# Performance work log

Measured on AMD Instinct MI355X. Metric: run time of the kernel, lower is better.

## Reference

```python
import jax, jax.numpy as jnp
import numpy as np

B, L, D = 8, 4096, 512
KS = (3, 5, 7)
EPS = 1e-5
W_SCALE = 0.02  # tame torch.randn-style init for numerical sanity


def layernorm(x, g, b):
    mu = jnp.mean(x, axis=-1, keepdims=True)
    var = jnp.var(x, axis=-1, keepdims=True)
    return (x - mu) * jax.lax.rsqrt(var + EPS) * g + b


def masked_conv(x1, chain, W, b):
    # x1: (B, C, L); W: (O, C, K); chain: (B, L) int32
    K = W.shape[2]
    pad_l = (K - 1) // 2
    pad_r = (K - 1) - pad_l
    xp = jnp.pad(x1, ((0, 0), (0, 0), (pad_l, pad_r)))
    ip = jnp.pad(chain, ((0, 0), (pad_l, pad_r)))  # pad id = 0
    Lx = x1.shape[2]
    # center tap of each window is the position's own chain id (odd K, center == pad_l)
    out = b[None, :, None]
    for k in range(K):  # small static loop over taps
        xs = xp[:, :, k:k + Lx]                      # (B, C, L)
        mk = (ip[:, k:k + Lx] == chain)              # (B, L) bool
        out = out + jnp.einsum('bcl,oc->bol', xs * mk[:, None, :], W[:, :, k])
    return out


def setup_inputs() -> dict:
    key = jax.random.key(0)
    ks = jax.random.split(key, 16)
    inp = {
        'x': jax.random.normal(ks[0], (B, L, D), dtype=jnp.float32),
        'chain': jnp.sort(jax.random.randint(ks[1], (B, L), 0, 8), axis=-1).astype(jnp.int32),
    }
    for i, (name, K) in enumerate(zip(('W3', 'W5', 'W7'), KS)):
        inp[name] = jax.random.normal(ks[2 + i], (D, D, K), dtype=jnp.float32) * W_SCALE
        inp['b' + name[1:]] = jax.random.normal(ks[5 + i], (D,), dtype=jnp.float32) * W_SCALE
    inp['mlp_w1'] = jax.random.normal(ks[8], (D, 4 * D), dtype=jnp.float32) * W_SCALE
    inp['mlp_b1'] = jnp.zeros((4 * D,), dtype=jnp.float32)
    inp['mlp_w2'] = jax.random.normal(ks[9], (4 * D, D), dtype=jnp.float32) * W_SCALE
    inp['mlp_b2'] = jnp.zeros((D,), dtype=jnp.float32)
    inp['ln1_g'] = jnp.ones((D,), dtype=jnp.float32)
    inp['ln1_b'] = jnp.zeros((D,), dtype=jnp.float32)
    inp['ln2_g'] = jnp.ones((D,), dtype=jnp.float32)
    inp['ln2_b'] = jnp.zeros((D,), dtype=jnp.float32)
    return inp


def reference(x, chain, W3, b3, W5, b5, W7, b7,
              mlp_w1, mlp_b1, mlp_w2, mlp_b2,
              ln1_g, ln1_b, ln2_g, ln2_b):
    x1 = jnp.transpose(x, (0, 2, 1))  # (B, C, L)
    for W, b in ((W3, b3), (W5, b5), (W7, b7)):
        x1 = masked_conv(x1, chain, W, b)
    h = layernorm(x + jnp.transpose(x1, (0, 2, 1)), ln1_g, ln1_b)
    mlp = jax.nn.gelu(h @ mlp_w1 + mlp_b1) @ mlp_w2 + mlp_b2
    return layernorm(h + mlp, ln2_g, ln2_b)
```

## Files before the change

kernel.cpp:

```cpp
#include <hip/hip_runtime.h>
#include <math.h>

#define BB 8
#define LL 4096
#define DD 512
#define PTOT (BB*LL)
#define HID  2048

typedef __attribute__((ext_vector_type(8))) short short8;
typedef __attribute__((ext_vector_type(4))) float f32x4;

typedef __attribute__((address_space(1))) const unsigned int gconst_u32;
typedef __attribute__((address_space(3))) unsigned int lds_u32;

__device__ __forceinline__ void gload16(const void* g, void* l) {
    __builtin_amdgcn_global_load_lds((gconst_u32*)g, (lds_u32*)l, 16, 0, 0);
}

__device__ __forceinline__ unsigned short f2bf(float f) {
    union { float f; unsigned int u; } v; v.f = f;
    unsigned int r = v.u + 0x7fffu + ((v.u >> 16) & 1u);
    return (unsigned short)(r >> 16);
}
__device__ __forceinline__ float bf2f(unsigned short h) {
    union { unsigned int u; float f; } v; v.u = ((unsigned int)h) << 16;
    return v.f;
}
__device__ __forceinline__ float gelu_fast(float x) {
    float x2 = x * x;
    float t  = x * fmaf(0.044715f, x2, 1.0f);
    float e  = __builtin_amdgcn_exp2f(-2.3021143f * t);
    return x * __builtin_amdgcn_rcpf(1.0f + e);
}

__device__ __forceinline__ void barrier_sync() {
    asm volatile("" ::: "memory");
    __builtin_amdgcn_s_barrier();
    asm volatile("" ::: "memory");
}
#define WAITV(N) asm volatile("s_waitcnt vmcnt(" #N ")" ::: "memory")
#define WAITL0() asm volatile("s_waitcnt lgkmcnt(0)" ::: "memory")
#define SCHED0() __builtin_amdgcn_sched_barrier(0)

__global__ __launch_bounds__(256) void convert_x(const float* __restrict__ x,
                                                 unsigned short* __restrict__ xb,
                                                 unsigned short* __restrict__ zp) {
    int tid = blockIdx.x * 256 + threadIdx.x;
    if (blockIdx.x == 0 && threadIdx.x < 128) zp[threadIdx.x] = 0;
    float4 v = ((const float4*)x)[tid];
    uint2 o;
    o.x = (unsigned int)f2bf(v.x) | ((unsigned int)f2bf(v.y) << 16);
    o.y = (unsigned int)f2bf(v.z) | ((unsigned int)f2bf(v.w) << 16);
    ((uint2*)xb)[tid] = o;
}

__global__ __launch_bounds__(256) void trans_wconv(const float* __restrict__ W,
                                                   unsigned short* __restrict__ Wt, int K) {
    int tid = blockIdx.x * 256 + threadIdx.x;
    if (tid >= DD * DD * K) return;
    int o  = tid / (K * DD);
    int kc = tid - o * K * DD;
    int k  = kc >> 9;
    int c  = kc & (DD - 1);
    Wt[tid] = f2bf(W[(o * DD + c) * K + k]);
}

__global__ __launch_bounds__(256) void trans_w1(const float* __restrict__ W,
                                                unsigned short* __restrict__ Wt) {
    int tid = blockIdx.x * 256 + threadIdx.x;
    int n = tid >> 9;
    int c = tid & (DD - 1);
    Wt[tid] = f2bf(W[c * HID + n]);
}

__global__ __launch_bounds__(256) void trans_w2(const float* __restrict__ W,
                                                unsigned short* __restrict__ Wt) {
    int tid = blockIdx.x * 256 + threadIdx.x;
    int n = tid >> 11;
    int h = tid & (HID - 1);
    Wt[tid] = f2bf(W[h * DD + n]);
}

__global__ __launch_bounds__(256) void make_srcp(const int* __restrict__ chain,
                                                 int* __restrict__ srcp, int K) {
    int tid = blockIdx.x * 256 + threadIdx.x;
    if (tid >= PTOT * K) return;
    int p = tid / K;
    int k = tid - p * K;
    int b = p >> 12;
    int l = p & (LL - 1);
    int pad = (K - 1) >> 1;
    int l2 = l + k - pad;
    bool ok = (l2 >= 0) && (l2 < LL) && (chain[b * LL + l2] == chain[b * LL + l]);
    srcp[tid] = ok ? (p + k - pad) : -1;
}

template <int TAPS, int EPI>
__global__ __launch_bounds__(512) void mfma_gemm6(
        const unsigned short* __restrict__ A, int lda,
        const int* __restrict__ srcp,
        const unsigned short* __restrict__ Bt, int ldb,
        const float* __restrict__ bias,
        void* __restrict__ Yv, int ldc, int Kspan,
        const unsigned short* __restrict__ zp) {
    __shared__ alignas(16) unsigned short As[2 * 256 * 64];
    __shared__ alignas(16) unsigned short Bs[2 * 256 * 64];
    __shared__ int srcp_s[TAPS > 0 ? 256 * TAPS : 4];

    const int t = threadIdx.x;
    const int lane = t & 63, w = t >> 6;
    const int wr = w & 1, wc = w >> 1;
    const int lm = lane & 15, qh = lane >> 4, x7 = lane & 7;
    const int qq = (lane & 7) ^ (lane >> 3);
    const int l3 = lane >> 3;
    const int p0 = blockIdx.x * 256;
    const int o0 = blockIdx.y * 256;
    const int NKT = TAPS ? TAPS * 8 : (Kspan >> 6);

    f32x4 acc[8][4];
#pragma unroll
    for (int mi = 0; mi < 8; mi++)
#pragma unroll
        for (int nj = 0; nj < 4; nj++) acc[mi][nj] = (f32x4){0.f, 0.f, 0.f, 0.f};

    auto stgB = [&](int h) {
        if (h >= 4 * NKT) return;
        int jt = h >> 2;
        int rb = (h & 2) ? 128 : 0;
        unsigned short* dst = Bs + (jt & 1) * 16384 + (rb + w * 16) * 64;
        int kb = jt << 6;
#pragma unroll
        for (int i = 0; i < 2; i++) {
            int rl = rb + w * 16 + i * 8 + l3;
            gload16(Bt + (size_t)(o0 + rl) * ldb + kb + qq * 8, dst + i * 512);
        }
    };
    auto stgA = [&](int h, int sp0, int sp1) {
        if (h >= 4 * NKT) return;
        int jt = h >> 2;
        int rb = (h & 2) ? 128 : 0;
        unsigned short* dst = As + (jt & 1) * 16384 + (rb + w * 16) * 64;
#pragma unroll
        for (int i = 0; i < 2; i++) {
            const unsigned short* g;
            if (TAPS) {
                int sp = i ? sp1 : sp0;
                g = (sp >= 0) ? (A + (size_t)sp * lda + (jt & 7) * 64 + qq * 8) : zp;
            } else {
                int rl = rb + w * 16 + i * 8 + l3;
                g = A + (size_t)(p0 + rl) * lda + (jt << 6) + qq * 8;
            }
            gload16(g, dst + i * 512);
        }
    };
    auto ldsp = [&](int h, int& sp0, int& sp1) {
        if (TAPS && h < 4 * NKT) {
            int jt = h >> 2, tap = jt >> 3;
            int rb = (h & 2) ? 128 : 0;
            int rl = rb + w * 16 + l3;
            sp0 = srcp_s[rl * TAPS + tap];
            sp1 = srcp_s[(rl + 8) * TAPS + tap];
        }
    };

    if (TAPS) {
        for (int idx = t; idx < 256 * TAPS; idx += 512)
            srcp_s[idx] = srcp[(size_t)p0 * TAPS + idx];
    }
    __syncthreads();
    int sp0 = -1, sp1 = -1;
    ldsp(0, sp0, sp1); stgA(0, sp0, sp1);
    stgB(1);
    ldsp(2, sp0, sp1); stgA(2, sp0, sp1);
    stgB(3);
    ldsp(4, sp0, sp1); stgA(4, sp0, sp1);
    stgB(5);
    ldsp(6, sp0, sp1);
    WAITV(4);
    barrier_sync();

#define RD_A(MIH) do {                                                          \
    _Pragma("unroll")                                                           \
    for (int kk = 0; kk < 2; kk++) {                                            \
        int sa = ((kk * 4 + qh) ^ x7) * 8;                                      \
        _Pragma("unroll")                                                       \
        for (int m = 0; m < 4; m++)                                             \
            af[m][kk] = *(const short8*)&as_[((((MIH)*4+m)*2 + wr)*16 + lm)*64 + sa]; \
    } } while (0)
#define RD_B(NJH, BF) do {                                                      \
    _Pragma("unroll")                                                           \
    for (int kk = 0; kk < 2; kk++) {                                            \
        int sa = ((kk * 4 + qh) ^ x7) * 8;                                      \
        _Pragma("unroll")                                                       \
        for (int n = 0; n < 2; n++)                                             \
            BF[n][kk] = *(const short8*)&bs_[((((NJH)*2+n)*4 + wc)*16 + lm)*64 + sa]; \
    } } while (0)
#define MFMA_Q(MIH, NJH, BF)                                                    \
    __builtin_amdgcn_s_setprio(1);                                              \
    _Pragma("unroll")                                                           \
    for (int kk = 0; kk < 2; kk++)                                              \
        _Pragma("unroll")                                                       \
        for (int m = 0; m < 4; m++)                                             \
            _Pragma("unroll")                                                   \
            for (int n = 0; n < 2; n++)                                         \
                acc[(MIH)*4+m][(NJH)*2+n] = __builtin_amdgcn_mfma_f32_16x16x32_bf16( \
                    af[m][kk], BF[n][kk], acc[(MIH)*4+m][(NJH)*2+n], 0, 0, 0);  \
    __builtin_amdgcn_s_setprio(0)

    short8 af[4][2], bf0[2][2], bf1[2][2];
#pragma unroll 1
    for (int kt = 0; kt < NKT; ++kt) {
        const unsigned short* as_ = As + (kt & 1) * 16384;
        const unsigned short* bs_ = Bs + (kt & 1) * 16384;
        const bool last = (kt == NKT - 1);
        RD_A(0); RD_B(0, bf0); RD_B(1, bf1);
        if (!last) { stgA(4 * kt + 6, sp0, sp1); stgB(4 * kt + 7); }
        WAITL0(); SCHED0();
        MFMA_Q(0, 0, bf0);
        MFMA_Q(0, 1, bf1);
        if (!last) ldsp(4 * kt + 8, sp0, sp1);
        barrier_sync();
        RD_A(1);
        if (!last) { stgA(4 * kt + 8, sp0, sp1); stgB(4 * kt + 9); }
        WAITL0(); SCHED0();
        MFMA_Q(1, 0, bf0);
        MFMA_Q(1, 1, bf1);
        if (!last) ldsp(4 * kt + 10, sp0, sp1);
        if (kt == NKT - 2) { WAITV(0); } else if (!last) { WAITV(4); }
        barrier_sync();
    }
#undef RD_A
#undef RD_B
#undef MFMA_Q

#pragma unroll
    for (int mi = 0; mi < 8; mi++) {
#pragma unroll
        for (int nj = 0; nj < 4; nj++) {
            int col = o0 + (nj * 4 + wc) * 16 + lm;
#pragma unroll
            for (int r = 0; r < 4; r++) {
                int row = p0 + (mi * 2 + wr) * 16 + qh * 4 + r;
                float v = acc[mi][nj][r];
                size_t idx = (size_t)row * ldc + col;
                if (EPI == 0) {
                    ((unsigned short*)Yv)[idx] = f2bf(v + bias[col]);
                } else if (EPI == 1) {
                    ((unsigned short*)Yv)[idx] = f2bf(gelu_fast(v + bias[col]));
                } else if (EPI == 2) {
                    ((float*)Yv)[idx] = v + bias[col];
                } else {
                    ((float*)Yv)[idx] += v;
                }
            }
        }
    }
}

__global__ __launch_bounds__(256) void ln1_kernel(const float* __restrict__ x,
                                                  const unsigned short* __restrict__ conv,
                                                  const float* __restrict__ g,
                                                  const float* __restrict__ beta,
                                                  unsigned short* __restrict__ h) {
    int p = blockIdx.x, t = threadIdx.x;
    size_t base = (size_t)p * DD;
    float v0 = x[base + t] + bf2f(conv[base + t]);
    float v1 = x[base + 256 + t] + bf2f(conv[base + 256 + t]);
    float s = v0 + v1, sq = v0 * v0 + v1 * v1;
#pragma unroll
    for (int off = 32; off > 0; off >>= 1) { s += __shfl_xor(s, off); sq += __shfl_xor(sq, off); }
    __shared__ float red[2][4];
    int wid = t >> 6, lane = t & 63;
    if (lane == 0) { red[0][wid] = s; red[1][wid] = sq; }
    __syncthreads();
    float S = red[0][0] + red[0][1] + red[0][2] + red[0][3];
    float SQ = red[1][0] + red[1][1] + red[1][2] + red[1][3];
    float mu = S * (1.f / DD);
    float var = SQ * (1.f / DD) - mu * mu;
    float rs = rsqrtf(var + 1e-5f);
    h[base + t]       = f2bf((v0 - mu) * rs * g[t] + beta[t]);
    h[base + 256 + t] = f2bf((v1 - mu) * rs * g[256 + t] + beta[256 + t]);
}

__global__ __launch_bounds__(256) void ln2_kernel(const unsigned short* __restrict__ h,
                                                  float* __restrict__ out,
                                                  const float* __restrict__ g,
                                                  const float* __restrict__ beta) {
    int p = blockIdx.x, t = threadIdx.x;
    size_t base = (size_t)p * DD;
    float v0 = bf2f(h[base + t]) + out[base + t];
    float v1 = bf2f(h[base + 256 + t]) + out[base + 256 + t];
    float s = v0 + v1, sq = v0 * v0 + v1 * v1;
#pragma unroll
    for (int off = 32; off > 0; off >>= 1) { s += __shfl_xor(s, off); sq += __shfl_xor(sq, off); }
    __shared__ float red[2][4];
    int wid = t >> 6, lane = t & 63;
    if (lane == 0) { red[0][wid] = s; red[1][wid] = sq; }
    __syncthreads();
    float S = red[0][0] + red[0][1] + red[0][2] + red[0][3];
    float SQ = red[1][0] + red[1][1] + red[1][2] + red[1][3];
    float mu = S * (1.f / DD);
    float var = SQ * (1.f / DD) - mu * mu;
    float rs = rsqrtf(var + 1e-5f);
    out[base + t]       = (v0 - mu) * rs * g[t] + beta[t];
    out[base + 256 + t] = (v1 - mu) * rs * g[256 + t] + beta[256 + t];
}

extern "C" void kernel_launch(void* const* d_in, const int* in_sizes, int n_in,
                              void* d_out, int out_size, void* d_ws, size_t ws_size,
                              hipStream_t stream) {
    const float* x     = (const float*)d_in[0];
    const int*   chain = (const int*)d_in[1];
    const float* W3    = (const float*)d_in[2];
    const float* b3    = (const float*)d_in[3];
    const float* W5    = (const float*)d_in[4];
    const float* b5    = (const float*)d_in[5];
    const float* W7    = (const float*)d_in[6];
    const float* b7    = (const float*)d_in[7];
    const float* w1    = (const float*)d_in[8];
    const float* bm1   = (const float*)d_in[9];
    const float* w2    = (const float*)d_in[10];
    const float* bm2   = (const float*)d_in[11];
    const float* g1    = (const float*)d_in[12];
    const float* be1   = (const float*)d_in[13];
    const float* g2    = (const float*)d_in[14];
    const float* be2   = (const float*)d_in[15];
    float* out = (float*)d_out;

    const size_t ACT = (size_t)PTOT * DD * 2;
    char* ws = (char*)d_ws;
    size_t off = 0;
    unsigned short* Xb   = (unsigned short*)(ws + off); off += ACT;
    unsigned short* buf1 = (unsigned short*)(ws + off); off += ACT;
    unsigned short* buf2 = (unsigned short*)(ws + off); off += ACT;
    unsigned short* w3t  = (unsigned short*)(ws + off); off += (size_t)3 * DD * DD * 2;
    unsigned short* w5t  = (unsigned short*)(ws + off); off += (size_t)5 * DD * DD * 2;
    unsigned short* w7t  = (unsigned short*)(ws + off); off += (size_t)7 * DD * DD * 2;
    unsigned short* w1t  = (unsigned short*)(ws + off); off += (size_t)DD * HID * 2;
    unsigned short* w2t  = (unsigned short*)(ws + off); off += (size_t)DD * HID * 2;
    int* srcp3 = (int*)(ws + off); off += (size_t)PTOT * 3 * 4;
    int* srcp5 = (int*)(ws + off); off += (size_t)PTOT * 5 * 4;
    int* srcp7 = (int*)(ws + off); off += (size_t)PTOT * 7 * 4;
    unsigned short* zp = (unsigned short*)(ws + off); off += 256;
    size_t base_off = off;
    bool full = (ws_size >= base_off + (size_t)PTOT * HID * 2);
    unsigned short* Hb = (unsigned short*)(ws + base_off);

    convert_x<<<PTOT * DD / (256 * 4), 256, 0, stream>>>(x, Xb, zp);
    trans_wconv<<<(DD * DD * 3 + 255) / 256, 256, 0, stream>>>(W3, w3t, 3);
    trans_wconv<<<(DD * DD * 5 + 255) / 256, 256, 0, stream>>>(W5, w5t, 5);
    trans_wconv<<<(DD * DD * 7 + 255) / 256, 256, 0, stream>>>(W7, w7t, 7);
    trans_w1<<<DD * HID / 256, 256, 0, stream>>>(w1, w1t);
    trans_w2<<<DD * HID / 256, 256, 0, stream>>>(w2, w2t);
    make_srcp<<<(PTOT * 3 + 255) / 256, 256, 0, stream>>>(chain, srcp3, 3);
    make_srcp<<<(PTOT * 5 + 255) / 256, 256, 0, stream>>>(chain, srcp5, 5);
    make_srcp<<<(PTOT * 7 + 255) / 256, 256, 0, stream>>>(chain, srcp7, 7);

    dim3 gconv(PTOT / 256, DD / 256);

    mfma_gemm6<3, 0><<<gconv, 512, 0, stream>>>(Xb, DD, srcp3, w3t, 3 * DD, b3, buf1, DD, DD, zp);
    mfma_gemm6<5, 0><<<gconv, 512, 0, stream>>>(buf1, DD, srcp5, w5t, 5 * DD, b5, buf2, DD, DD, zp);
    mfma_gemm6<7, 0><<<gconv, 512, 0, stream>>>(buf2, DD, srcp7, w7t, 7 * DD, b7, buf1, DD, DD, zp);

    ln1_kernel<<<PTOT, 256, 0, stream>>>(x, buf1, g1, be1, buf2);

    if (full) {
        dim3 g1d(PTOT / 256, HID / 256);
        mfma_gemm6<0, 1><<<g1d, 512, 0, stream>>>(buf2, DD, nullptr, w1t, DD, bm1,
                                                  Hb, HID, DD, zp);
        mfma_gemm6<0, 2><<<gconv, 512, 0, stream>>>(Hb, HID, nullptr, w2t, HID, bm2,
                                                    out, DD, HID, zp);
    } else {
        for (int jc = 0; jc < 4; jc++) {
            mfma_gemm6<0, 1><<<gconv, 512, 0, stream>>>(buf2, DD, nullptr,
                                                        w1t + (size_t)jc * DD * DD, DD,
                                                        bm1 + jc * DD, Hb, DD, DD, zp);
            if (jc == 0)
                mfma_gemm6<0, 2><<<gconv, 512, 0, stream>>>(Hb, DD, nullptr,
                                                            w2t + jc * DD, HID, bm2,
                                                            out, DD, DD, zp);
            else
                mfma_gemm6<0, 3><<<gconv, 512, 0, stream>>>(Hb, DD, nullptr,
                                                            w2t + jc * DD, HID, bm2,
                                                            out, DD, DD, zp);
        }
    }

    ln2_kernel<<<PTOT, 256, 0, stream>>>(buf2, out, g2, be2);
}
```

Before: 652.7 us.

## Deepen GEMM prefetch pipeline and preload next-tile LDS fragments before barrier

Restructures the main MFMA GEMM loop so the first A/B fragments of the next k-tile are read from LDS at the end of each iteration, letting MFMAs start right after the barrier. Global-to-LDS staging now issues all four stages of the next tile at once, with a deeper vmcnt wait (8 outstanding loads instead of 4). The aim is to hide LDS read latency and global-load latency behind the MFMAs. In exchange it uses more registers for the extra srcp indices and relies on subtle barrier and wait-count correctness around the double-buffered LDS.

```diff
diff --git a/kernel.cpp b/kernel.cpp
--- a/kernel.cpp
+++ b/kernel.cpp
@@ -96,7 +96,7 @@
 }
 
 template <int TAPS, int EPI>
-__global__ __launch_bounds__(512) void mfma_gemm6(
+__global__ __launch_bounds__(512) void mfma_gemm8(
         const unsigned short* __restrict__ A, int lda,
         const int* __restrict__ srcp,
         const unsigned short* __restrict__ Bt, int ldb,
@@ -168,34 +168,31 @@
             srcp_s[idx] = srcp[(size_t)p0 * TAPS + idx];
     }
     __syncthreads();
-    int sp0 = -1, sp1 = -1;
-    ldsp(0, sp0, sp1); stgA(0, sp0, sp1);
-    stgB(1);
-    ldsp(2, sp0, sp1); stgA(2, sp0, sp1);
-    stgB(3);
-    ldsp(4, sp0, sp1); stgA(4, sp0, sp1);
-    stgB(5);
-    ldsp(6, sp0, sp1);
-    WAITV(4);
+    int sp0 = -1, sp1 = -1, sp2 = -1, sp3 = -1;
+    ldsp(0, sp0, sp1); stgA(0, sp0, sp1); stgB(1);
+    ldsp(2, sp0, sp1); stgA(2, sp0, sp1); stgB(3);
+    ldsp(4, sp0, sp1); stgA(4, sp0, sp1); stgB(5);
+    ldsp(6, sp0, sp1); stgA(6, sp0, sp1); stgB(7);
+    WAITV(8);
     barrier_sync();
 
-#define RD_A(MIH) do {                                                          \
+#define RD_A(AF, MIH, BASE) do {                                                \
     _Pragma("unroll")                                                           \
     for (int kk = 0; kk < 2; kk++) {                                            \
         int sa = ((kk * 4 + qh) ^ x7) * 8;                                      \
         _Pragma("unroll")                                                       \
         for (int m = 0; m < 4; m++)                                             \
-            af[m][kk] = *(const short8*)&as_[((((MIH)*4+m)*2 + wr)*16 + lm)*64 + sa]; \
+            AF[m][kk] = *(const short8*)&(BASE)[((((MIH)*4+m)*2 + wr)*16 + lm)*64 + sa]; \
     } } while (0)
-#define RD_B(NJH, BF) do {                                                      \
+#define RD_B(BF, NJH, BASE) do {                                                \
     _Pragma("unroll")                                                           \
     for (int kk = 0; kk < 2; kk++) {                                            \
         int sa = ((kk * 4 + qh) ^ x7) * 8;                                      \
         _Pragma("unroll")                                                       \
         for (int n = 0; n < 2; n++)                                             \
-            BF[n][kk] = *(const short8*)&bs_[((((NJH)*2+n)*4 + wc)*16 + lm)*64 + sa]; \
+            BF[n][kk] = *(const short8*)&(BASE)[((((NJH)*2+n)*4 + wc)*16 + lm)*64 + sa]; \
     } } while (0)
-#define MFMA_Q(MIH, NJH, BF)                                                    \
+#define MFMA_Q(AF, MIH, BF, NJH)                                                \
     __builtin_amdgcn_s_setprio(1);                                              \
     _Pragma("unroll")                                                           \
     for (int kk = 0; kk < 2; kk++)                                              \
@@ -204,29 +201,45 @@
             _Pragma("unroll")                                                   \
             for (int n = 0; n < 2; n++)                                         \
                 acc[(MIH)*4+m][(NJH)*2+n] = __builtin_amdgcn_mfma_f32_16x16x32_bf16( \
-                    af[m][kk], BF[n][kk], acc[(MIH)*4+m][(NJH)*2+n], 0, 0, 0);  \
+                    AF[m][kk], BF[n][kk], acc[(MIH)*4+m][(NJH)*2+n], 0, 0, 0);  \
     __builtin_amdgcn_s_setprio(0)
 
     short8 af[4][2], bf0[2][2], bf1[2][2];
+    RD_A(af, 0, As);
+    RD_B(bf0, 0, Bs);
+
 #pragma unroll 1
     for (int kt = 0; kt < NKT; ++kt) {
-        const unsigned short* as_ = As + (kt & 1) * 16384;
-        const unsigned short* bs_ = Bs + (kt & 1) * 16384;
+        const unsigned short* as_  = As + (kt & 1) * 16384;
+        const unsigned short* bs_  = Bs + (kt & 1) * 16384;
+        const unsigned short* as2_ = As + ((kt + 1) & 1) * 16384;
+        const unsigned short* bs2_ = Bs + ((kt + 1) & 1) * 16384;
         const bool last = (kt == NKT - 1);
-        RD_A(0); RD_B(0, bf0); RD_B(1, bf1);
-        if (!last) { stgA(4 * kt + 6, sp0, sp1); stgB(4 * kt + 7); }
-        WAITL0(); SCHED0();
-        MFMA_Q(0, 0, bf0);
-        MFMA_Q(0, 1, bf1);
-        if (!last) ldsp(4 * kt + 8, sp0, sp1);
+        RD_B(bf1, 1, bs_);
+        MFMA_Q(af, 0, bf0, 0);
+        MFMA_Q(af, 0, bf1, 1);
+        SCHED0();
+        RD_A(af, 1, as_);
+        if (!last) {
+            ldsp(4 * kt + 8, sp0, sp1);
+            ldsp(4 * kt + 10, sp2, sp3);
+            WAITV(4);
+        }
+        WAITL0();
         barrier_sync();
-        RD_A(1);
-        if (!last) { stgA(4 * kt + 8, sp0, sp1); stgB(4 * kt + 9); }
-        WAITL0(); SCHED0();
-        MFMA_Q(1, 0, bf0);
-        MFMA_Q(1, 1, bf1);
-        if (!last) ldsp(4 * kt + 10, sp0, sp1);
-        if (kt == NKT - 2) { WAITV(0); } else if (!last) { WAITV(4); }
+        MFMA_Q(af, 1, bf0, 0);
+        MFMA_Q(af, 1, bf1, 1);
+        SCHED0();
+        if (!last) {
+            RD_A(af, 0, as2_);
+            RD_B(bf0, 0, bs2_);
+            stgA(4 * kt + 8, sp0, sp1);
+            stgB(4 * kt + 9);
+            stgA(4 * kt + 10, sp2, sp3);
+            stgB(4 * kt + 11);
+            if (kt == NKT - 2) { WAITV(0); } else { WAITV(8); }
+        }
+        WAITL0();
         barrier_sync();
     }
 #undef RD_A
@@ -358,29 +371,29 @@
 
     dim3 gconv(PTOT / 256, DD / 256);
 
-    mfma_gemm6<3, 0><<<gconv, 512, 0, stream>>>(Xb, DD, srcp3, w3t, 3 * DD, b3, buf1, DD, DD, zp);
-    mfma_gemm6<5, 0><<<gconv, 512, 0, stream>>>(buf1, DD, srcp5, w5t, 5 * DD, b5, buf2, DD, DD, zp);
-    mfma_gemm6<7, 0><<<gconv, 512, 0, stream>>>(buf2, DD, srcp7, w7t, 7 * DD, b7, buf1, DD, DD, zp);
+    mfma_gemm8<3, 0><<<gconv, 512, 0, stream>>>(Xb, DD, srcp3, w3t, 3 * DD, b3, buf1, DD, DD, zp);
+    mfma_gemm8<5, 0><<<gconv, 512, 0, stream>>>(buf1, DD, srcp5, w5t, 5 * DD, b5, buf2, DD, DD, zp);
+    mfma_gemm8<7, 0><<<gconv, 512, 0, stream>>>(buf2, DD, srcp7, w7t, 7 * DD, b7, buf1, DD, DD, zp);
 
     ln1_kernel<<<PTOT, 256, 0, stream>>>(x, buf1, g1, be1, buf2);
 
     if (full) {
         dim3 g1d(PTOT / 256, HID / 256);
-        mfma_gemm6<0, 1><<<g1d, 512, 0, stream>>>(buf2, DD, nullptr, w1t, DD, bm1,
+        mfma_gemm8<0, 1><<<g1d, 512, 0, stream>>>(buf2, DD, nullptr, w1t, DD, bm1,
                                                   Hb, HID, DD, zp);
-        mfma_gemm6<0, 2><<<gconv, 512, 0, stream>>>(Hb, HID, nullptr, w2t, HID, bm2,
+        mfma_gemm8<0, 2><<<gconv, 512, 0, stream>>>(Hb, HID, nullptr, w2t, HID, bm2,
                                                     out, DD, HID, zp);
     } else {
         for (int jc = 0; jc < 4; jc++) {
-            mfma_gemm6<0, 1><<<gconv, 512, 0, stream>>>(buf2, DD, nullptr,
+            mfma_gemm8<0, 1><<<gconv, 512, 0, stream>>>(buf2, DD, nullptr,
                                                         w1t + (size_t)jc * DD * DD, DD,
                                                         bm1 + jc * DD, Hb, DD, DD, zp);
             if (jc == 0)
-                mfma_gemm6<0, 2><<<gconv, 512, 0, stream>>>(Hb, DD, nullptr,
+                mfma_gemm8<0, 2><<<gconv, 512, 0, stream>>>(Hb, DD, nullptr,
                                                             w2t + jc * DD, HID, bm2,
                                                             out, DD, DD, zp);
             else
-                mfma_gemm6<0, 3><<<gconv, 512, 0, stream>>>(Hb, DD, nullptr,
+                mfma_gemm8<0, 3><<<gconv, 512, 0, stream>>>(Hb, DD, nullptr,
                                                             w2t + jc * DD, HID, bm2,
                                                             out, DD, DD, zp);
         }
```

New measurement: 673.3 us. 3.2% more time.
